# Performance work log

Hardware: AMD Instinct MI355X
Metric: run time of the kernel (lower is better)

## Reference

```python
import jax, jax.numpy as jnp
import numpy as np

WH, WW = 7, 7
N = WH * WW            # 49 tokens per window
DIM = 128
HEADS = 4
HEAD_DIM = DIM // HEADS
SCALE = HEAD_DIM ** -0.5
NW = 1024              # windows per image (224/7)^2
B = 16                 # images
B_ = B * NW


def _relative_position_index():
    ch, cw = np.meshgrid(np.arange(WH), np.arange(WW), indexing='ij')
    coords = np.stack([ch, cw]).reshape(2, -1)          # [2, N]
    rel = coords[:, :, None] - coords[:, None, :]        # [2, N, N]
    rel = rel.transpose(1, 2, 0)
    rel[:, :, 0] += WH - 1
    rel[:, :, 1] += WW - 1
    rel[:, :, 0] *= 2 * WW - 1
    return rel.sum(-1).astype(np.int32)                 # [N, N]


def setup_inputs() -> dict:
    key = jax.random.key(0)
    ks = jax.random.split(key, 5)
    x = jax.random.normal(ks[0], (B_, N, DIM), dtype=jnp.float32)
    mask = jnp.zeros((NW, N, N), dtype=jnp.float32)
    qkv_w = jax.random.normal(ks[1], (3 * DIM, DIM), dtype=jnp.float32) * (DIM ** -0.5)
    qkv_b = jnp.zeros((3 * DIM,), dtype=jnp.float32)
    proj_w = jax.random.normal(ks[2], (DIM, DIM), dtype=jnp.float32) * (DIM ** -0.5)
    proj_b = jnp.zeros((DIM,), dtype=jnp.float32)
    rel_bias_table = jax.random.normal(ks[3], ((2 * WH - 1) * (2 * WW - 1), HEADS), dtype=jnp.float32) * 0.02
    rel_index = jnp.asarray(_relative_position_index())
    return {"x": x, "mask": mask, "qkv_w": qkv_w, "qkv_b": qkv_b,
            "proj_w": proj_w, "proj_b": proj_b,
            "rel_bias_table": rel_bias_table, "rel_index": rel_index}


def reference(x, mask, qkv_w, qkv_b, proj_w, proj_b, rel_bias_table, rel_index):
    Bw, n, c = x.shape
    # fused qkv projection: [B_, N, 3, H, hd]
    qkv = (x @ qkv_w.T + qkv_b).reshape(Bw, n, 3, HEADS, HEAD_DIM)
    qkv = jnp.transpose(qkv, (2, 0, 3, 1, 4))            # [3, B_, H, N, hd]
    q, k, v = qkv[0], qkv[1], qkv[2]
    attn = jnp.einsum('bhnd,bhmd->bhnm', q * SCALE, k)   # [B_, H, N, N]
    # gathered relative position bias: [N, N, H] -> [H, N, N]
    bias = rel_bias_table[rel_index.reshape(-1)].reshape(n, n, HEADS)
    attn = attn + jnp.transpose(bias, (2, 0, 1))[None]
    # additive per-window mask
    nW = mask.shape[0]
    attn = attn.reshape(Bw // nW, nW, HEADS, n, n) + mask[None, :, None]
    attn = jax.nn.softmax(attn.reshape(Bw, HEADS, n, n), axis=-1)
    out = jnp.einsum('bhnm,bhmd->bhnd', attn, v)         # [B_, H, N, hd]
    out = jnp.transpose(out, (0, 2, 1, 3)).reshape(Bw, n, c)
    return out @ proj_w.T + proj_b
```

## Files before the change

kernel.cpp:

```cpp
#include <hip/hip_runtime.h>
#include <hip/hip_bf16.h>


#define NTOK 49
#define DIMC 128
#define HEADS 4
#define NWM  1024
#define SCALE 0.17677669529663687f

typedef __attribute__((ext_vector_type(8))) __bf16 bf16x8;
typedef __attribute__((ext_vector_type(4))) float f32x4;

#define OFF_Q  0
#define OFF_K  12544
#define OFF_P  0
#define OFF_XB 25088
#define OFF_VT 25088
#define OFF_AO 25088
#define SMEM_BYTES 39440

__device__ __forceinline__ unsigned short f2bf(float f) {
  union { float f; unsigned u; } x; x.f = f;
  unsigned r = x.u + 0x7fffu + ((x.u >> 16) & 1u);
  return (unsigned short)(r >> 16);
}

__device__ __forceinline__ f32x4 mfma16(bf16x8 a, bf16x8 b, f32x4 c) {
  return __builtin_amdgcn_mfma_f32_16x16x32_bf16(a, b, c, 0, 0, 0);
}

__device__ __forceinline__ bf16x8 zero8() {
  bf16x8 z;
#pragma unroll
  for (int j = 0; j < 8; ++j) z[j] = (__bf16)0.f;
  return z;
}

__global__ void winattn_prep(const float* __restrict__ qkv_w,
                             const float* __restrict__ proj_w,
                             const float* __restrict__ table,
                             const int* __restrict__ ridx,
                             unsigned short* __restrict__ qkv_wb,
                             unsigned short* __restrict__ proj_wb,
                             float* __restrict__ bias_g) {
  int i = blockIdx.x * 256 + threadIdx.x;
  if (i < 384 * DIMC) qkv_wb[i] = f2bf(qkv_w[i]);
  if (i < DIMC * DIMC) proj_wb[i] = f2bf(proj_w[i]);
  if (i < HEADS * 64 * 64) {
    int h = i >> 12, n = (i >> 6) & 63, m = i & 63;
    float v = -1e30f;
    if (n < NTOK && m < NTOK) v = table[ridx[n * NTOK + m] * HEADS + h];
    bias_g[i] = v;
  }
}

__launch_bounds__(256, 4)
__global__ void winattn_main(const float* __restrict__ x,
                             const float* __restrict__ mask,
                             const unsigned short* __restrict__ qkv_wb,
                             const float* __restrict__ qkv_b,
                             const unsigned short* __restrict__ proj_wb,
                             const float* __restrict__ proj_b,
                             const float* __restrict__ bias_g,
                             float* __restrict__ out) {
  __shared__ char smem[SMEM_BYTES] __attribute__((aligned(128)));
  const int tid  = threadIdx.x;
  const int w    = blockIdx.x;
  const int lane = tid & 63;
  const int wid  = tid >> 6;
  const int lr   = lane & 15;
  const int lg   = lane >> 4;
  const f32x4 fzero = {0.f, 0.f, 0.f, 0.f};

  const float* xw = x + (size_t)w * (NTOK * DIMC);

  for (int i = tid; i < NTOK * 16; i += 256) {
    int n = i >> 4, c8 = i & 15;
    float4 v0 = *reinterpret_cast<const float4*>(xw + n * DIMC + c8 * 8);
    float4 v1 = *reinterpret_cast<const float4*>(xw + n * DIMC + c8 * 8 + 4);
    uint4 d;
    d.x = (unsigned)f2bf(v0.x) | ((unsigned)f2bf(v0.y) << 16);
    d.y = (unsigned)f2bf(v0.z) | ((unsigned)f2bf(v0.w) << 16);
    d.z = (unsigned)f2bf(v1.x) | ((unsigned)f2bf(v1.y) << 16);
    d.w = (unsigned)f2bf(v1.z) | ((unsigned)f2bf(v1.w) << 16);
    int mb = (c8 * 16) ^ ((n & 7) << 4);
    *reinterpret_cast<uint4*>(smem + OFF_XB + n * 256 + mb) = d;
  }
  if (tid == 0)
    *reinterpret_cast<uint4*>(smem + SMEM_BYTES - 16) = make_uint4(0u, 0u, 0u, 0u);
  __syncthreads();

  bf16x8 af[4][4];
#pragma unroll
  for (int mt = 0; mt < 4; ++mt)
#pragma unroll
    for (int kk = 0; kk < 4; ++kk) {
      int n = mt * 16 + lr;
      bool pad = (n > 48);
      if (pad) n = 48;
      int mb = (kk * 64 + 16 * lg) ^ ((n & 7) << 4);
      bf16x8 v = *reinterpret_cast<const bf16x8*>(smem + OFF_XB + n * 256 + mb);
      af[mt][kk] = pad ? zero8() : v;
    }
  __syncthreads();

  {
    const int cb = wid * 96;
#pragma unroll
    for (int nt = 0; nt < 6; ++nt) {
      const int o = cb + nt * 16 + lr;
      const unsigned short* wrow = qkv_wb + o * DIMC;
      bf16x8 bf[4];
#pragma unroll
      for (int kk = 0; kk < 4; ++kk)
        bf[kk] = *reinterpret_cast<const bf16x8*>(wrow + kk * 32 + lg * 8);
      f32x4 acc[4];
#pragma unroll
      for (int mt = 0; mt < 4; ++mt) acc[mt] = fzero;
#pragma unroll
      for (int kk = 0; kk < 4; ++kk)
#pragma unroll
        for (int mt = 0; mt < 4; ++mt)
          acc[mt] = mfma16(af[mt][kk], bf[kk], acc[mt]);
      const float bq = qkv_b[o];
      const int s  = o >> 7;
      const int h2 = (o & 127) >> 5;
      const int d  = o & 31;
#pragma unroll
      for (int mt = 0; mt < 4; ++mt)
#pragma unroll
        for (int r = 0; r < 4; ++r) {
          const int n = mt * 16 + lg * 4 + r;
          const unsigned short bv = f2bf(acc[mt][r] + bq);
          if (s == 2) {
            if (n < 56)
              *reinterpret_cast<unsigned short*>(
                  smem + OFF_VT + (h2 * 32 + d) * 112 + n * 2) = bv;
          } else if (n < NTOK) {
            int base = (s == 0) ? OFF_Q : OFF_K;
            int mb = (d * 2) ^ ((n & 3) << 4);
            *reinterpret_cast<unsigned short*>(
                smem + base + (h2 * NTOK + n) * 64 + mb) = bv;
          }
        }
    }
  }
  __syncthreads();

  const int h = wid;
  {
    bf16x8 qf[4], kf[4];
#pragma unroll
    for (int mt = 0; mt < 4; ++mt) {
      int n = mt * 16 + lr; if (n > 48) n = 48;
      int mb = (lg * 16) ^ ((n & 3) << 4);
      qf[mt] = *reinterpret_cast<const bf16x8*>(smem + OFF_Q + (h * NTOK + n) * 64 + mb);
    }
#pragma unroll
    for (int nt = 0; nt < 4; ++nt) {
      int m = nt * 16 + lr; if (m > 48) m = 48;
      int mb = (lg * 16) ^ ((m & 3) << 4);
      kf[nt] = *reinterpret_cast<const bf16x8*>(smem + OFF_K + (h * NTOK + m) * 64 + mb);
    }
    f32x4 sc[4][4];
#pragma unroll
    for (int mt = 0; mt < 4; ++mt)
#pragma unroll
      for (int nt = 0; nt < 4; ++nt)
        sc[mt][nt] = mfma16(qf[mt], kf[nt], fzero);

    const float* bgh = bias_g + h * 4096;
    const float* mw  = mask + (size_t)(w & (NWM - 1)) * (NTOK * NTOK);
#pragma unroll
    for (int mt = 0; mt < 4; ++mt)
#pragma unroll
      for (int r = 0; r < 4; ++r) {
        const int n  = mt * 16 + lg * 4 + r;
        const int nc = (n > 48) ? 48 : n;
#pragma unroll
        for (int nt = 0; nt < 4; ++nt) {
          const int m  = nt * 16 + lr;
          const int mc = (m > 48) ? 48 : m;
          sc[mt][nt][r] = sc[mt][nt][r] * SCALE + bgh[n * 64 + m] + mw[nc * NTOK + mc];
        }
      }
    __syncthreads();

#pragma unroll
    for (int mt = 0; mt < 4; ++mt)
#pragma unroll
      for (int r = 0; r < 4; ++r) {
        float mx = sc[mt][0][r];
#pragma unroll
        for (int nt = 1; nt < 4; ++nt) mx = fmaxf(mx, sc[mt][nt][r]);
        mx = fmaxf(mx, __shfl_xor(mx, 1, 16));
        mx = fmaxf(mx, __shfl_xor(mx, 2, 16));
        mx = fmaxf(mx, __shfl_xor(mx, 4, 16));
        mx = fmaxf(mx, __shfl_xor(mx, 8, 16));
        float e[4]; float sum = 0.f;
#pragma unroll
        for (int nt = 0; nt < 4; ++nt) { e[nt] = __expf(sc[mt][nt][r] - mx); sum += e[nt]; }
        sum += __shfl_xor(sum, 1, 16);
        sum += __shfl_xor(sum, 2, 16);
        sum += __shfl_xor(sum, 4, 16);
        sum += __shfl_xor(sum, 8, 16);
        const float inv = __builtin_amdgcn_rcpf(sum);
        const int n = mt * 16 + lg * 4 + r;
        if (n < NTOK) {
#pragma unroll
          for (int nt = 0; nt < 4; ++nt) {
            const int m = nt * 16 + lr;
            int mb = (m * 2) ^ ((n & 7) << 4);
            *reinterpret_cast<unsigned short*>(smem + OFF_P + (h * NTOK + n) * 128 + mb) =
                f2bf(e[nt] * inv);
          }
        }
      }
  }

  {
    bf16x8 pa[4][2], vb[2][2];
#pragma unroll
    for (int mt = 0; mt < 4; ++mt)
#pragma unroll
      for (int kk = 0; kk < 2; ++kk) {
        int n = mt * 16 + lr; if (n > 48) n = 48;
        int mb = (kk * 64 + lg * 16) ^ ((n & 7) << 4);
        pa[mt][kk] = *reinterpret_cast<const bf16x8*>(smem + OFF_P + (h * NTOK + n) * 128 + mb);
      }
#pragma unroll
    for (int dt = 0; dt < 2; ++dt)
#pragma unroll
      for (int kk = 0; kk < 2; ++kk) {
        const int d = dt * 16 + lr;
        vb[dt][kk] = *reinterpret_cast<const bf16x8*>(
            smem + OFF_VT + (h * 32 + d) * 112 + kk * 64 + 16 * lg);
      }
    f32x4 oc[4][2];
#pragma unroll
    for (int mt = 0; mt < 4; ++mt)
#pragma unroll
      for (int dt = 0; dt < 2; ++dt) oc[mt][dt] = fzero;
#pragma unroll
    for (int kk = 0; kk < 2; ++kk)
#pragma unroll
      for (int mt = 0; mt < 4; ++mt)
#pragma unroll
        for (int dt = 0; dt < 2; ++dt)
          oc[mt][dt] = mfma16(pa[mt][kk], vb[dt][kk], oc[mt][dt]);
    __syncthreads();
#pragma unroll
    for (int mt = 0; mt < 4; ++mt)
#pragma unroll
      for (int dt = 0; dt < 2; ++dt)
#pragma unroll
        for (int r = 0; r < 4; ++r) {
          const int n = mt * 16 + lg * 4 + r;
          if (n < NTOK) {
            const int c = h * 32 + dt * 16 + lr;
            int mb = (c * 2) ^ ((n & 7) << 4);
            *reinterpret_cast<unsigned short*>(smem + OFF_AO + n * 256 + mb) =
                f2bf(oc[mt][dt][r]);
          }
        }
  }
  __syncthreads();

  {
    bf16x8 aof[4][4];
#pragma unroll
    for (int mt = 0; mt < 4; ++mt)
#pragma unroll
      for (int kk = 0; kk < 4; ++kk) {
        int n = mt * 16 + lr; if (n > 48) n = 48;
        int s16 = 4 * kk + lg;
        aof[mt][kk] = *reinterpret_cast<const bf16x8*>(
            smem + OFF_AO + n * 256 + (((s16 & 8) | ((s16 ^ (n & 7)) & 7)) << 4));
      }
    float* ow = out + (size_t)w * (NTOK * DIMC);
#pragma unroll
    for (int ct = 0; ct < 2; ++ct) {
      const int c = (wid * 2 + ct) * 16 + lr;
      const unsigned short* wrow = proj_wb + c * DIMC;
      bf16x8 wb[4];
#pragma unroll
      for (int kk = 0; kk < 4; ++kk)
        wb[kk] = *reinterpret_cast<const bf16x8*>(wrow + kk * 32 + lg * 8);
      f32x4 acc[4];
#pragma unroll
      for (int mt = 0; mt < 4; ++mt) acc[mt] = fzero;
#pragma unroll
      for (int kk = 0; kk < 4; ++kk)
#pragma unroll
        for (int mt = 0; mt < 4; ++mt)
          acc[mt] = mfma16(aof[mt][kk], wb[kk], acc[mt]);
      const float bp = proj_b[c];
#pragma unroll
      for (int mt = 0; mt < 4; ++mt)
#pragma unroll
        for (int r = 0; r < 4; ++r) {
          const int n = mt * 16 + lg * 4 + r;
          if (n < NTOK) ow[n * DIMC + c] = acc[mt][r] + bp;
        }
    }
  }
}

extern "C" void kernel_launch(void* const* d_in, const int* in_sizes, int n_in,
                              void* d_out, int out_size, void* d_ws, size_t ws_size,
                              hipStream_t stream) {
  const float* x      = (const float*)d_in[0];
  const float* mask   = (const float*)d_in[1];
  const float* qkv_w  = (const float*)d_in[2];
  const float* qkv_b  = (const float*)d_in[3];
  const float* proj_w = (const float*)d_in[4];
  const float* proj_b = (const float*)d_in[5];
  const float* table  = (const float*)d_in[6];
  const int*   ridx   = (const int*)d_in[7];

  unsigned short* qkv_wb  = (unsigned short*)d_ws;
  unsigned short* proj_wb = qkv_wb + 384 * DIMC;
  float*          bias_g  = (float*)(proj_wb + DIMC * DIMC);

  winattn_prep<<<192, 256, 0, stream>>>(qkv_w, proj_w, table, ridx,
                                        qkv_wb, proj_wb, bias_g);

  const int nwin = in_sizes[0] / (NTOK * DIMC);
  winattn_main<<<nwin, 256, 0, stream>>>(x, mask, qkv_wb, qkv_b, proj_wb,
                                         proj_b, bias_g, (float*)d_out);
}
```

Measured before the change: 549.1 us.

## Swap MFMA operand order so outputs land contiguous, enabling vectorized stores

Swaps the A and B operands of the MFMAs in the Q/K projection, P·V and output projection. Each lane then holds 4 consecutive output channels for one token, so the scattered 2-byte LDS stores and scalar 4-byte global stores become packed uint2 LDS stores and float4 global stores. It also uses the packed hardware bf16 conversion in place of manual rounding, and reassigns QKV output tiles so each wave produces its own head's Q/K/V. The global store pattern changes from per-column scalar writes to 16-byte row chunks, which should cut store instruction count and LDS bank traffic.

```diff
diff --git a/kernel.cpp b/kernel.cpp
--- a/kernel.cpp
+++ b/kernel.cpp
@@ -23,6 +23,12 @@
   union { float f; unsigned u; } x; x.f = f;
   unsigned r = x.u + 0x7fffu + ((x.u >> 16) & 1u);
   return (unsigned short)(r >> 16);
+}
+
+__device__ __forceinline__ unsigned pk2(float a, float b) {
+  __hip_bfloat162 t = __float22bfloat162_rn(make_float2(a, b));
+  union { __hip_bfloat162 h; unsigned u; } c; c.h = t;
+  return c.u;
 }
 
 __device__ __forceinline__ f32x4 mfma16(bf16x8 a, bf16x8 b, f32x4 c) {
@@ -79,10 +85,10 @@
     float4 v0 = *reinterpret_cast<const float4*>(xw + n * DIMC + c8 * 8);
     float4 v1 = *reinterpret_cast<const float4*>(xw + n * DIMC + c8 * 8 + 4);
     uint4 d;
-    d.x = (unsigned)f2bf(v0.x) | ((unsigned)f2bf(v0.y) << 16);
-    d.y = (unsigned)f2bf(v0.z) | ((unsigned)f2bf(v0.w) << 16);
-    d.z = (unsigned)f2bf(v1.x) | ((unsigned)f2bf(v1.y) << 16);
-    d.w = (unsigned)f2bf(v1.z) | ((unsigned)f2bf(v1.w) << 16);
+    d.x = pk2(v0.x, v0.y);
+    d.y = pk2(v0.z, v0.w);
+    d.z = pk2(v1.x, v1.y);
+    d.w = pk2(v1.z, v1.w);
     int mb = (c8 * 16) ^ ((n & 7) << 4);
     *reinterpret_cast<uint4*>(smem + OFF_XB + n * 256 + mb) = d;
   }
@@ -104,45 +110,58 @@
     }
   __syncthreads();
 
-  {
-    const int cb = wid * 96;
-#pragma unroll
-    for (int nt = 0; nt < 6; ++nt) {
-      const int o = cb + nt * 16 + lr;
-      const unsigned short* wrow = qkv_wb + o * DIMC;
-      bf16x8 bf[4];
+#pragma unroll
+  for (int t = 0; t < 6; ++t) {
+    const int sec  = t >> 1;
+    const int half = t & 1;
+    const int o0   = sec * 128 + 32 * wid + 16 * half;
+    const unsigned short* wrow = qkv_wb + (o0 + lr) * DIMC;
+    bf16x8 wf[4];
+#pragma unroll
+    for (int kk = 0; kk < 4; ++kk)
+      wf[kk] = *reinterpret_cast<const bf16x8*>(wrow + kk * 32 + 8 * lg);
+    f32x4 acc[4];
+#pragma unroll
+    for (int mt = 0; mt < 4; ++mt) acc[mt] = fzero;
+    if (sec < 2) {
 #pragma unroll
       for (int kk = 0; kk < 4; ++kk)
-        bf[kk] = *reinterpret_cast<const bf16x8*>(wrow + kk * 32 + lg * 8);
-      f32x4 acc[4];
-#pragma unroll
-      for (int mt = 0; mt < 4; ++mt) acc[mt] = fzero;
+#pragma unroll
+        for (int mt = 0; mt < 4; ++mt)
+          acc[mt] = mfma16(wf[kk], af[mt][kk], acc[mt]);
+      float4 bq = *reinterpret_cast<const float4*>(qkv_b + o0 + 4 * lg);
+      const int base = (sec == 0) ? OFF_Q : OFF_K;
+      const int d0x2 = 32 * half + 8 * lg;
+#pragma unroll
+      for (int mt = 0; mt < 4; ++mt) {
+        int n = mt * 16 + lr;
+        if (n < NTOK) {
+          unsigned lo = pk2(acc[mt][0] + bq.x, acc[mt][1] + bq.y);
+          unsigned hi = pk2(acc[mt][2] + bq.z, acc[mt][3] + bq.w);
+          int byte = (wid * NTOK + n) * 64 + (d0x2 ^ ((n & 3) << 4));
+          *reinterpret_cast<uint2*>(smem + base + byte) = make_uint2(lo, hi);
+        }
+      }
+    } else {
 #pragma unroll
       for (int kk = 0; kk < 4; ++kk)
 #pragma unroll
         for (int mt = 0; mt < 4; ++mt)
-          acc[mt] = mfma16(af[mt][kk], bf[kk], acc[mt]);
-      const float bq = qkv_b[o];
-      const int s  = o >> 7;
-      const int h2 = (o & 127) >> 5;
-      const int d  = o & 31;
-#pragma unroll
-      for (int mt = 0; mt < 4; ++mt)
-#pragma unroll
-        for (int r = 0; r < 4; ++r) {
-          const int n = mt * 16 + lg * 4 + r;
-          const unsigned short bv = f2bf(acc[mt][r] + bq);
-          if (s == 2) {
-            if (n < 56)
-              *reinterpret_cast<unsigned short*>(
-                  smem + OFF_VT + (h2 * 32 + d) * 112 + n * 2) = bv;
-          } else if (n < NTOK) {
-            int base = (s == 0) ? OFF_Q : OFF_K;
-            int mb = (d * 2) ^ ((n & 3) << 4);
-            *reinterpret_cast<unsigned short*>(
-                smem + base + (h2 * NTOK + n) * 64 + mb) = bv;
-          }
-        }
+          acc[mt] = mfma16(af[mt][kk], wf[kk], acc[mt]);
+      float bq = qkv_b[o0 + lr];
+      int d = 16 * half + lr;
+      char* vrow = smem + OFF_VT + (wid * 32 + d) * 112;
+#pragma unroll
+      for (int mt = 0; mt < 4; ++mt) {
+        int n0 = mt * 16 + 4 * lg;
+        if (n0 <= 48) {
+          unsigned lo = pk2(acc[mt][0] + bq, acc[mt][1] + bq);
+          unsigned hi = pk2(acc[mt][2] + bq, acc[mt][3] + bq);
+          *reinterpret_cast<uint2*>(vrow + n0 * 2) = make_uint2(lo, hi);
+        } else if (n0 == 52) {
+          *reinterpret_cast<uint2*>(vrow + 104) = make_uint2(0u, 0u);
+        }
+      }
     }
   }
   __syncthreads();
@@ -221,12 +240,12 @@
   {
     bf16x8 pa[4][2], vb[2][2];
 #pragma unroll
-    for (int mt = 0; mt < 4; ++mt)
+    for (int nt = 0; nt < 4; ++nt)
 #pragma unroll
       for (int kk = 0; kk < 2; ++kk) {
-        int n = mt * 16 + lr; if (n > 48) n = 48;
+        int n = nt * 16 + lr; if (n > 48) n = 48;
         int mb = (kk * 64 + lg * 16) ^ ((n & 7) << 4);
-        pa[mt][kk] = *reinterpret_cast<const bf16x8*>(smem + OFF_P + (h * NTOK + n) * 128 + mb);
+        pa[nt][kk] = *reinterpret_cast<const bf16x8*>(smem + OFF_P + (h * NTOK + n) * 128 + mb);
       }
 #pragma unroll
     for (int dt = 0; dt < 2; ++dt)
@@ -236,72 +255,74 @@
         vb[dt][kk] = *reinterpret_cast<const bf16x8*>(
             smem + OFF_VT + (h * 32 + d) * 112 + kk * 64 + 16 * lg);
       }
-    f32x4 oc[4][2];
-#pragma unroll
-    for (int mt = 0; mt < 4; ++mt)
-#pragma unroll
-      for (int dt = 0; dt < 2; ++dt) oc[mt][dt] = fzero;
+    f32x4 oc[2][4];
+#pragma unroll
+    for (int dt = 0; dt < 2; ++dt)
+#pragma unroll
+      for (int nt = 0; nt < 4; ++nt) oc[dt][nt] = fzero;
 #pragma unroll
     for (int kk = 0; kk < 2; ++kk)
 #pragma unroll
-      for (int mt = 0; mt < 4; ++mt)
-#pragma unroll
-        for (int dt = 0; dt < 2; ++dt)
-          oc[mt][dt] = mfma16(pa[mt][kk], vb[dt][kk], oc[mt][dt]);
+      for (int dt = 0; dt < 2; ++dt)
+#pragma unroll
+        for (int nt = 0; nt < 4; ++nt)
+          oc[dt][nt] = mfma16(vb[dt][kk], pa[nt][kk], oc[dt][nt]);
     __syncthreads();
 #pragma unroll
-    for (int mt = 0; mt < 4; ++mt)
-#pragma unroll
-      for (int dt = 0; dt < 2; ++dt)
-#pragma unroll
-        for (int r = 0; r < 4; ++r) {
-          const int n = mt * 16 + lg * 4 + r;
-          if (n < NTOK) {
-            const int c = h * 32 + dt * 16 + lr;
-            int mb = (c * 2) ^ ((n & 7) << 4);
-            *reinterpret_cast<unsigned short*>(smem + OFF_AO + n * 256 + mb) =
-                f2bf(oc[mt][dt][r]);
-          }
-        }
+    for (int dt = 0; dt < 2; ++dt)
+#pragma unroll
+      for (int nt = 0; nt < 4; ++nt) {
+        int n = nt * 16 + lr;
+        if (n < NTOK) {
+          unsigned lo = pk2(oc[dt][nt][0], oc[dt][nt][1]);
+          unsigned hi = pk2(oc[dt][nt][2], oc[dt][nt][3]);
+          int c0x2 = 64 * h + 32 * dt + 8 * lg;
+          int byte = n * 256 + (c0x2 ^ ((n & 7) << 4));
+          *reinterpret_cast<uint2*>(smem + OFF_AO + byte) = make_uint2(lo, hi);
+        }
+      }
   }
   __syncthreads();
 
   {
     bf16x8 aof[4][4];
 #pragma unroll
-    for (int mt = 0; mt < 4; ++mt)
+    for (int nt = 0; nt < 4; ++nt)
 #pragma unroll
       for (int kk = 0; kk < 4; ++kk) {
-        int n = mt * 16 + lr; if (n > 48) n = 48;
+        int n = nt * 16 + lr; if (n > 48) n = 48;
         int s16 = 4 * kk + lg;
-        aof[mt][kk] = *reinterpret_cast<const bf16x8*>(
+        aof[nt][kk] = *reinterpret_cast<const bf16x8*>(
             smem + OFF_AO + n * 256 + (((s16 & 8) | ((s16 ^ (n & 7)) & 7)) << 4));
       }
     float* ow = out + (size_t)w * (NTOK * DIMC);
 #pragma unroll
     for (int ct = 0; ct < 2; ++ct) {
-      const int c = (wid * 2 + ct) * 16 + lr;
-      const unsigned short* wrow = proj_wb + c * DIMC;
-      bf16x8 wb[4];
+      const int c0s = (wid * 2 + ct) * 16;
+      const unsigned short* wrow = proj_wb + (c0s + lr) * DIMC;
+      bf16x8 wf2[4];
 #pragma unroll
       for (int kk = 0; kk < 4; ++kk)
-        wb[kk] = *reinterpret_cast<const bf16x8*>(wrow + kk * 32 + lg * 8);
+        wf2[kk] = *reinterpret_cast<const bf16x8*>(wrow + kk * 32 + lg * 8);
       f32x4 acc[4];
 #pragma unroll
-      for (int mt = 0; mt < 4; ++mt) acc[mt] = fzero;
+      for (int nt = 0; nt < 4; ++nt) acc[nt] = fzero;
 #pragma unroll
       for (int kk = 0; kk < 4; ++kk)
 #pragma unroll
-        for (int mt = 0; mt < 4; ++mt)
-          acc[mt] = mfma16(aof[mt][kk], wb[kk], acc[mt]);
-      const float bp = proj_b[c];
-#pragma unroll
-      for (int mt = 0; mt < 4; ++mt)
-#pragma unroll
-        for (int r = 0; r < 4; ++r) {
-          const int n = mt * 16 + lg * 4 + r;
-          if (n < NTOK) ow[n * DIMC + c] = acc[mt][r] + bp;
-        }
+        for (int nt = 0; nt < 4; ++nt)
+          acc[nt] = mfma16(wf2[kk], aof[nt][kk], acc[nt]);
+      float4 bp = *reinterpret_cast<const float4*>(proj_b + c0s + 4 * lg);
+#pragma unroll
+      for (int nt = 0; nt < 4; ++nt) {
+        int n = nt * 16 + lr;
+        if (n < NTOK) {
+          float4 o;
+          o.x = acc[nt][0] + bp.x; o.y = acc[nt][1] + bp.y;
+          o.z = acc[nt][2] + bp.z; o.w = acc[nt][3] + bp.w;
+          *reinterpret_cast<float4*>(ow + n * DIMC + c0s + 4 * lg) = o;
+        }
+      }
     }
   }
 }
```

Result: slower. 630.6 us (+14.8%).

## Compute transposed scores and build P fragments in registers via lane shuffles

Applied to the files above, without the earlier changes.

The QK^T MFMA now swaps operands to produce transposed scores, so softmax reductions run along rows held within each lane plus two cross-lane shuffles. Bias and mask loads become vectorised float4 reads. Probabilities are packed to bf16 pairs and redistributed into PV A-operand fragments with wave shuffles, which removes the LDS write/read of P and the barrier before softmax. The extra shuffles and live registers led to relaxing launch bounds from 4 to 2 blocks per SM, which may lower occupancy.

```diff
diff --git a/kernel.cpp b/kernel.cpp
--- a/kernel.cpp
+++ b/kernel.cpp
@@ -13,7 +13,6 @@
 
 #define OFF_Q  0
 #define OFF_K  12544
-#define OFF_P  0
 #define OFF_XB 25088
 #define OFF_VT 25088
 #define OFF_AO 25088
@@ -23,6 +22,12 @@
   union { float f; unsigned u; } x; x.f = f;
   unsigned r = x.u + 0x7fffu + ((x.u >> 16) & 1u);
   return (unsigned short)(r >> 16);
+}
+
+__device__ __forceinline__ unsigned pk2(float a, float b) {
+  __hip_bfloat162 t = __float22bfloat162_rn(make_float2(a, b));
+  union { __hip_bfloat162 h; unsigned u; } c; c.h = t;
+  return c.u;
 }
 
 __device__ __forceinline__ f32x4 mfma16(bf16x8 a, bf16x8 b, f32x4 c) {
@@ -54,7 +59,7 @@
   }
 }
 
-__launch_bounds__(256, 4)
+__launch_bounds__(256, 2)
 __global__ void winattn_main(const float* __restrict__ x,
                              const float* __restrict__ mask,
                              const unsigned short* __restrict__ qkv_wb,
@@ -148,6 +153,7 @@
   __syncthreads();
 
   const int h = wid;
+  bf16x8 pa[4][2];
   {
     bf16x8 qf[4], kf[4];
 #pragma unroll
@@ -164,70 +170,88 @@
     }
     f32x4 sc[4][4];
 #pragma unroll
-    for (int mt = 0; mt < 4; ++mt)
-#pragma unroll
-      for (int nt = 0; nt < 4; ++nt)
-        sc[mt][nt] = mfma16(qf[mt], kf[nt], fzero);
+    for (int mi = 0; mi < 4; ++mi)
+#pragma unroll
+      for (int ni = 0; ni < 4; ++ni)
+        sc[mi][ni] = mfma16(kf[mi], qf[ni], fzero);
 
     const float* bgh = bias_g + h * 4096;
     const float* mw  = mask + (size_t)(w & (NWM - 1)) * (NTOK * NTOK);
 #pragma unroll
-    for (int mt = 0; mt < 4; ++mt)
-#pragma unroll
-      for (int r = 0; r < 4; ++r) {
-        const int n  = mt * 16 + lg * 4 + r;
+    for (int mi = 0; mi < 4; ++mi) {
+      const int m0 = mi * 16 + lg * 4;
+#pragma unroll
+      for (int ni = 0; ni < 4; ++ni) {
+        const int n  = ni * 16 + lr;
         const int nc = (n > 48) ? 48 : n;
-#pragma unroll
-        for (int nt = 0; nt < 4; ++nt) {
-          const int m  = nt * 16 + lr;
-          const int mc = (m > 48) ? 48 : m;
-          sc[mt][nt][r] = sc[mt][nt][r] * SCALE + bgh[n * 64 + m] + mw[nc * NTOK + mc];
-        }
-      }
-    __syncthreads();
-
-#pragma unroll
-    for (int mt = 0; mt < 4; ++mt)
-#pragma unroll
-      for (int r = 0; r < 4; ++r) {
-        float mx = sc[mt][0][r];
-#pragma unroll
-        for (int nt = 1; nt < 4; ++nt) mx = fmaxf(mx, sc[mt][nt][r]);
-        mx = fmaxf(mx, __shfl_xor(mx, 1, 16));
-        mx = fmaxf(mx, __shfl_xor(mx, 2, 16));
-        mx = fmaxf(mx, __shfl_xor(mx, 4, 16));
-        mx = fmaxf(mx, __shfl_xor(mx, 8, 16));
-        float e[4]; float sum = 0.f;
-#pragma unroll
-        for (int nt = 0; nt < 4; ++nt) { e[nt] = __expf(sc[mt][nt][r] - mx); sum += e[nt]; }
-        sum += __shfl_xor(sum, 1, 16);
-        sum += __shfl_xor(sum, 2, 16);
-        sum += __shfl_xor(sum, 4, 16);
-        sum += __shfl_xor(sum, 8, 16);
-        const float inv = __builtin_amdgcn_rcpf(sum);
-        const int n = mt * 16 + lg * 4 + r;
-        if (n < NTOK) {
-#pragma unroll
-          for (int nt = 0; nt < 4; ++nt) {
-            const int m = nt * 16 + lr;
-            int mb = (m * 2) ^ ((n & 7) << 4);
-            *reinterpret_cast<unsigned short*>(smem + OFF_P + (h * NTOK + n) * 128 + mb) =
-                f2bf(e[nt] * inv);
-          }
-        }
+        float4 bg = *reinterpret_cast<const float4*>(bgh + n * 64 + m0);
+        float4 mk;
+        if (mi < 3) {
+          mk.x = mw[nc * NTOK + m0];     mk.y = mw[nc * NTOK + m0 + 1];
+          mk.z = mw[nc * NTOK + m0 + 2]; mk.w = mw[nc * NTOK + m0 + 3];
+        } else {
+          float ms = mw[nc * NTOK + 48];
+          mk.x = ms; mk.y = ms; mk.z = ms; mk.w = ms;
+        }
+        sc[mi][ni][0] = sc[mi][ni][0] * SCALE + bg.x + mk.x;
+        sc[mi][ni][1] = sc[mi][ni][1] * SCALE + bg.y + mk.y;
+        sc[mi][ni][2] = sc[mi][ni][2] * SCALE + bg.z + mk.z;
+        sc[mi][ni][3] = sc[mi][ni][3] * SCALE + bg.w + mk.w;
+      }
+    }
+    uint2 pk[4][4];
+#pragma unroll
+    for (int ni = 0; ni < 4; ++ni) {
+      float mx = sc[0][ni][0];
+#pragma unroll
+      for (int mi = 0; mi < 4; ++mi)
+#pragma unroll
+        for (int r = 0; r < 4; ++r) mx = fmaxf(mx, sc[mi][ni][r]);
+      mx = fmaxf(mx, __shfl_xor(mx, 16));
+      mx = fmaxf(mx, __shfl_xor(mx, 32));
+      float sum = 0.f;
+#pragma unroll
+      for (int mi = 0; mi < 4; ++mi)
+#pragma unroll
+        for (int r = 0; r < 4; ++r) {
+          sc[mi][ni][r] = __expf(sc[mi][ni][r] - mx);
+          sum += sc[mi][ni][r];
+        }
+      sum += __shfl_xor(sum, 16);
+      sum += __shfl_xor(sum, 32);
+      const float inv = __builtin_amdgcn_rcpf(sum);
+#pragma unroll
+      for (int mi = 0; mi < 4; ++mi) {
+        pk[mi][ni].x = pk2(sc[mi][ni][0] * inv, sc[mi][ni][1] * inv);
+        pk[mi][ni].y = pk2(sc[mi][ni][2] * inv, sc[mi][ni][3] * inv);
+      }
+    }
+    const int srcLow  = lr + ((lg & 1) ? 32 : 0);
+    const int srcHigh = srcLow + 16;
+    const bool hiSel  = (lg >> 1) != 0;
+#pragma unroll
+    for (int ni = 0; ni < 4; ++ni)
+#pragma unroll
+      for (int kk = 0; kk < 2; ++kk) {
+        unsigned a0x = __shfl(pk[kk * 2][ni].x, srcLow);
+        unsigned a0y = __shfl(pk[kk * 2][ni].y, srcLow);
+        unsigned a1x = __shfl(pk[kk * 2 + 1][ni].x, srcLow);
+        unsigned a1y = __shfl(pk[kk * 2 + 1][ni].y, srcLow);
+        unsigned b0x = __shfl(pk[kk * 2][ni].x, srcHigh);
+        unsigned b0y = __shfl(pk[kk * 2][ni].y, srcHigh);
+        unsigned b1x = __shfl(pk[kk * 2 + 1][ni].x, srcHigh);
+        unsigned b1y = __shfl(pk[kk * 2 + 1][ni].y, srcHigh);
+        union { uint4 u; bf16x8 b; } cvt;
+        cvt.u.x = hiSel ? a1x : a0x;
+        cvt.u.y = hiSel ? a1y : a0y;
+        cvt.u.z = hiSel ? b1x : b0x;
+        cvt.u.w = hiSel ? b1y : b0y;
+        pa[ni][kk] = cvt.b;
       }
   }
 
   {
-    bf16x8 pa[4][2], vb[2][2];
-#pragma unroll
-    for (int mt = 0; mt < 4; ++mt)
-#pragma unroll
-      for (int kk = 0; kk < 2; ++kk) {
-        int n = mt * 16 + lr; if (n > 48) n = 48;
-        int mb = (kk * 64 + lg * 16) ^ ((n & 7) << 4);
-        pa[mt][kk] = *reinterpret_cast<const bf16x8*>(smem + OFF_P + (h * NTOK + n) * 128 + mb);
-      }
+    bf16x8 vb[2][2];
 #pragma unroll
     for (int dt = 0; dt < 2; ++dt)
 #pragma unroll
```

Result: slower. 654.3 us (+19.2%).
